# Kernel tuning notes

Measured on AMD Instinct MI355X. Metric: run time of the kernel, lower is better.

## Reference

```python
import jax, jax.numpy as jnp
import numpy as np

MEL_BINS = 128
NUM_KEYS = 88
FMAX = 8000.0
HPS_HARMONICS = 3
Q = 0.85  # threshold_percentile / 100


def _mel_frequencies(n_mels, fmin=0.0, fmax=FMAX):
    # Replicates librosa.mel_frequencies (Slaney scale, htk=False)
    f_sp = 200.0 / 3.0
    min_log_hz = 1000.0
    min_log_mel = min_log_hz / f_sp
    logstep = np.log(6.4) / 27.0

    def hz_to_mel(f):
        f = np.asarray(f, dtype=np.float64)
        lin = f / f_sp
        log = min_log_mel + np.log(np.maximum(f, 1e-12) / min_log_hz) / logstep
        return np.where(f >= min_log_hz, log, lin)

    def mel_to_hz(m):
        m = np.asarray(m, dtype=np.float64)
        lin = f_sp * m
        log = min_log_hz * np.exp(logstep * (m - min_log_mel))
        return np.where(m >= min_log_mel, log, lin)

    mels = np.linspace(hz_to_mel(fmin), hz_to_mel(fmax), n_mels)
    return mel_to_hz(mels)


def _compute_key_bins():
    mel_freqs = _mel_frequencies(MEL_BINS)
    bins = []
    for k in range(NUM_KEYS):
        freq = 440.0 * 2.0 ** ((k + 21 - 69) / 12.0)
        bin_idx = int(np.argmin(np.abs(mel_freqs - freq)))
        bins.append(min(bin_idx, MEL_BINS - 1))
    return np.asarray(bins, dtype=np.int64)


def setup_inputs() -> dict:
    key = jax.random.key(0)
    mel = jax.random.normal(key, (32, MEL_BINS, 8192), dtype=jnp.float32)
    key_bins = jnp.asarray(_compute_key_bins())
    return {"mel": mel, "key_bins": key_bins}


def reference(mel, key_bins):
    # mel: [B, MEL_BINS, T]
    spec = jnp.exp(mel)
    hps = spec
    for h in range(2, HPS_HARMONICS + 1):
        down = spec[:, ::h, :]          # [B, ceil(MEL_BINS/h), T]
        L = down.shape[1]
        hps = hps.at[:, :L, :].multiply(down)
    key_energies = hps[:, key_bins, :]  # [B, K, T]
    B, K, T = key_energies.shape
    flat = key_energies.transpose(0, 2, 1).reshape(B * T, K)
    thresh = jnp.quantile(flat, Q, axis=1, keepdims=True)  # linear interp, matches torch.quantile
    probs = (flat >= thresh).astype(jnp.float32).reshape(B, T, K).transpose(0, 2, 1)
    return (probs, probs)
```

## Files before the change

kernel.cpp:

```cpp
#include <hip/hip_runtime.h>
#include <math.h>

namespace {
constexpr int kB    = 32;
constexpr int kMel  = 128;
constexpr int kT    = 8192;
constexpr int kKeys = 88;
constexpr int kTop  = 15;
constexpr int kD    = 57;

constexpr int kDistM[kD] = {
    1,  2,  3,  4,  5,  6,  7,  8,  9, 10, 11, 12, 13, 14, 15, 16, 17,
   19, 20, 21, 22, 23, 25, 26, 28, 29, 31, 33, 35, 37, 39, 42,
   44, 46, 49, 51, 53, 56, 58, 60, 63, 65, 68, 70, 72, 75, 77, 79,
   82, 84, 86, 89, 91, 93, 96, 98, 101};
constexpr int kCnt[kD] = {
    5, 9, 6, 4, 3, 3, 3, 2, 2, 2, 1, 2, 1, 1, 1, 1, 2,
    1, 1, 1, 1, 1, 1, 1, 1, 1, 1, 1, 1, 1, 1, 1,
    1, 1, 1, 1, 1, 1, 1, 1, 1, 1, 1, 1, 1, 1, 1, 1,
    1, 1, 1, 1, 1, 1, 1, 1, 1};
constexpr int kIdx[kKeys] = {
    0, 0, 0, 0, 0,
    1, 1, 1, 1, 1, 1, 1, 1, 1,
    2, 2, 2, 2, 2, 2,
    3, 3, 3, 3,
    4, 4, 4,
    5, 5, 5,
    6, 6, 6,
    7, 7,
    8, 8,
    9, 9,
   10,
   11, 11,
   12, 13, 14, 15,
   16, 16,
   17, 18, 19, 20, 21, 22, 23, 24, 25, 26, 27, 28, 29, 30, 31,
   32, 33, 34, 35, 36, 37, 38, 39, 40, 41, 42, 43, 44, 45, 46, 47,
   48, 49, 50, 51, 52, 53, 54, 55, 56};
}

__device__ __forceinline__ void top_insert(float (&top)[kTop], float v) {
#pragma unroll
  for (int j = 0; j < kTop; ++j) {
    const float hi = fmaxf(top[j], v);
    v = fminf(top[j], v);
    top[j] = hi;
  }
}

__global__ __launch_bounds__(256, 4) void key_probs_kernel(
    const float* __restrict__ mel, const int* __restrict__ key_bins,
    float* __restrict__ out) {
  __shared__ int sbins[kKeys];
  const int tid = threadIdx.x;
  int ok = 1;
  if (tid < kKeys) {
    const int bin = key_bins[tid];
    sbins[tid] = bin;
    ok = (bin == kDistM[kIdx[tid]]);
  }
  const int allok = __syncthreads_and(ok);

  const int t = blockIdx.x * 256 + tid;
  const int b = blockIdx.y;
  const float* melb = mel + (size_t)b * kMel * kT + t;
  float* o0 = out + (size_t)b * kKeys * kT + t;
  float* o1 = o0 + (size_t)kB * kKeys * kT;

  if (allok) {
    float sd[kD];
#pragma unroll
    for (int j = 0; j < kD; ++j) {
      const int m = kDistM[j];
      float v = melb[(size_t)m * kT];
      if (2 * m < kMel) v += melb[(size_t)(2 * m) * kT];
      if (3 * m < kMel) v += melb[(size_t)(3 * m) * kT];
      sd[j] = v;
    }

    float top[kTop];
#pragma unroll
    for (int j = 0; j < kTop; ++j) top[j] = -1e30f;
#pragma unroll
    for (int j = 0; j < kD; ++j) {
#pragma unroll
      for (int c = 0; c < kCnt[j]; ++c) top_insert(top, sd[j]);
    }

    float r74 = top[13];
    const float vstar = top[13];

    int neq = 0;
    bool near_ne = false;
#pragma unroll
    for (int j = 0; j < kD; ++j) {
      const float d = sd[j] - vstar;
      const bool c = fabsf(d) < 1e-5f;
      near_ne = near_ne || (c && (d != 0.0f));
      neq += (c && (d == 0.0f)) ? 1 : 0;
    }
    const bool amb = near_ne || (neq > 1);

    if (amb) {
      float tp[kTop];
#pragma unroll
      for (int j = 0; j < kTop; ++j) tp[j] = 0.0f;
#pragma unroll
      for (int j = 0; j < kD; ++j) {
        const int m = kDistM[j];
        float v = (float)::exp((double)melb[(size_t)m * kT]);
        if (2 * m < kMel) v *= (float)::exp((double)melb[(size_t)(2 * m) * kT]);
        if (3 * m < kMel) v *= (float)::exp((double)melb[(size_t)(3 * m) * kT]);
        sd[j] = v;
#pragma unroll
        for (int c = 0; c < kCnt[j]; ++c) top_insert(tp, v);
      }
      r74 = tp[13];
    }

#pragma unroll
    for (int k = 0; k < kKeys; ++k) {
      const float r = (sd[kIdx[k]] >= r74) ? 1.0f : 0.0f;
      __builtin_nontemporal_store(r, &o0[(size_t)k * kT]);
      __builtin_nontemporal_store(r, &o1[(size_t)k * kT]);
    }
    return;
  }

  float s[kKeys];
#pragma unroll
  for (int k = 0; k < kKeys; ++k) {
    const int m = __builtin_amdgcn_readfirstlane(sbins[k]);
    const int r1 = (m < 64) ? 2 * m : m;
    const int r2 = (m < 43) ? 3 * m : m;
    const float w1 = (m < 64) ? 1.0f : 0.0f;
    const float w2 = (m < 43) ? 1.0f : 0.0f;
    const float v0 = melb[(size_t)m * kT];
    const float v1 = melb[(size_t)r1 * kT];
    const float v2 = melb[(size_t)r2 * kT];
    s[k] = v0 + w1 * v1 + w2 * v2;
  }

  float top[kTop];
#pragma unroll
  for (int j = 0; j < kTop; ++j) top[j] = -1e30f;
#pragma unroll
  for (int k = 0; k < kKeys; ++k) top_insert(top, s[k]);

  float r74 = top[13];
  const float vstar = top[13];

  bool tieok = true;
  int bmin = 0x3fffffff;
  int bmax = -0x3fffffff;
#pragma unroll
  for (int k = 0; k < kKeys; ++k) {
    const int m = __builtin_amdgcn_readfirstlane(sbins[k]);
    const float d = s[k] - vstar;
    const bool c = fabsf(d) < 1e-5f;
    tieok = tieok && (!c || (d == 0.0f));
    bmin = (c && m < bmin) ? m : bmin;
    bmax = (c && m > bmax) ? m : bmax;
  }
  const bool amb = !(tieok && (bmin == bmax));

  if (amb) {
    float tp[kTop];
#pragma unroll
    for (int j = 0; j < kTop; ++j) tp[j] = 0.0f;
#pragma unroll
    for (int k = 0; k < kKeys; ++k) {
      const int m = __builtin_amdgcn_readfirstlane(sbins[k]);
      float v = (float)::exp((double)melb[(size_t)m * kT]);
      if (m < 64) v *= (float)::exp((double)melb[(size_t)(2 * m) * kT]);
      if (m < 43) v *= (float)::exp((double)melb[(size_t)(3 * m) * kT]);
      s[k] = v;
      top_insert(tp, v);
    }
    r74 = tp[13];
  }

#pragma unroll
  for (int k = 0; k < kKeys; ++k) {
    const float r = (s[k] >= r74) ? 1.0f : 0.0f;
    __builtin_nontemporal_store(r, &o0[(size_t)k * kT]);
    __builtin_nontemporal_store(r, &o1[(size_t)k * kT]);
  }
}

extern "C" void kernel_launch(void* const* d_in, const int* in_sizes, int n_in,
                              void* d_out, int out_size, void* d_ws, size_t ws_size,
                              hipStream_t stream) {
  const float* mel = (const float*)d_in[0];
  const int* key_bins = (const int*)d_in[1];
  float* out = (float*)d_out;
  dim3 grid(kT / 256, kB);
  key_probs_kernel<<<grid, dim3(256), 0, stream>>>(mel, key_bins, out);
}
```

Baseline: 294.2 us.

## Pack threshold results with ballots into shared memory and emit vectorized float4 stores

Each wave now ballots its per-key comparison results into a shared bitmask table, and the block size grows to 1024 threads. After a block barrier, the threads expand the bits back into floats and write both output copies with 16-byte nontemporal vector stores, with each wave covering 11 output rows. This replaces per-thread 4-byte strided stores with wider stores, aiming at better write efficiency. The trade-offs are a block-wide sync and possibly lower occupancy from the 1024-thread blocks under heavy register use.

```diff
diff --git a/kernel.cpp b/kernel.cpp
--- a/kernel.cpp
+++ b/kernel.cpp
@@ -8,6 +8,12 @@
 constexpr int kKeys = 88;
 constexpr int kTop  = 15;
 constexpr int kD    = 57;
+
+constexpr int kThreads = 1024;
+constexpr int kWaves   = kThreads / 64;
+constexpr int kBlockT  = kThreads;
+
+typedef float floatx4 __attribute__((ext_vector_type(4)));
 
 constexpr int kDistM[kD] = {
     1,  2,  3,  4,  5,  6,  7,  8,  9, 10, 11, 12, 13, 14, 15, 16, 17,
@@ -48,10 +54,11 @@
   }
 }
 
-__global__ __launch_bounds__(256, 4) void key_probs_kernel(
+__global__ __launch_bounds__(kThreads, 1) void key_probs_kernel(
     const float* __restrict__ mel, const int* __restrict__ key_bins,
     float* __restrict__ out) {
   __shared__ int sbins[kKeys];
+  __shared__ unsigned long long fl[kKeys][kWaves];
   const int tid = threadIdx.x;
   int ok = 1;
   if (tid < kKeys) {
@@ -61,11 +68,10 @@
   }
   const int allok = __syncthreads_and(ok);
 
-  const int t = blockIdx.x * 256 + tid;
-  const int b = blockIdx.y;
-  const float* melb = mel + (size_t)b * kMel * kT + t;
-  float* o0 = out + (size_t)b * kKeys * kT + t;
-  float* o1 = o0 + (size_t)kB * kKeys * kT;
+  const int t0 = blockIdx.x * kBlockT;
+  const int b  = blockIdx.y;
+  const float* melb = mel + (size_t)b * kMel * kT + t0 + tid;
+  const int w = tid >> 6, lane = tid & 63;
 
   if (allok) {
     float sd[kD];
@@ -120,71 +126,91 @@
 
 #pragma unroll
     for (int k = 0; k < kKeys; ++k) {
-      const float r = (sd[kIdx[k]] >= r74) ? 1.0f : 0.0f;
-      __builtin_nontemporal_store(r, &o0[(size_t)k * kT]);
-      __builtin_nontemporal_store(r, &o1[(size_t)k * kT]);
-    }
-    return;
-  }
-
-  float s[kKeys];
-#pragma unroll
-  for (int k = 0; k < kKeys; ++k) {
-    const int m = __builtin_amdgcn_readfirstlane(sbins[k]);
-    const int r1 = (m < 64) ? 2 * m : m;
-    const int r2 = (m < 43) ? 3 * m : m;
-    const float w1 = (m < 64) ? 1.0f : 0.0f;
-    const float w2 = (m < 43) ? 1.0f : 0.0f;
-    const float v0 = melb[(size_t)m * kT];
-    const float v1 = melb[(size_t)r1 * kT];
-    const float v2 = melb[(size_t)r2 * kT];
-    s[k] = v0 + w1 * v1 + w2 * v2;
-  }
-
-  float top[kTop];
-#pragma unroll
-  for (int j = 0; j < kTop; ++j) top[j] = -1e30f;
-#pragma unroll
-  for (int k = 0; k < kKeys; ++k) top_insert(top, s[k]);
-
-  float r74 = top[13];
-  const float vstar = top[13];
-
-  bool tieok = true;
-  int bmin = 0x3fffffff;
-  int bmax = -0x3fffffff;
-#pragma unroll
-  for (int k = 0; k < kKeys; ++k) {
-    const int m = __builtin_amdgcn_readfirstlane(sbins[k]);
-    const float d = s[k] - vstar;
-    const bool c = fabsf(d) < 1e-5f;
-    tieok = tieok && (!c || (d == 0.0f));
-    bmin = (c && m < bmin) ? m : bmin;
-    bmax = (c && m > bmax) ? m : bmax;
-  }
-  const bool amb = !(tieok && (bmin == bmax));
-
-  if (amb) {
-    float tp[kTop];
-#pragma unroll
-    for (int j = 0; j < kTop; ++j) tp[j] = 0.0f;
+      const unsigned long long m = __ballot(sd[kIdx[k]] >= r74);
+      if (lane == 0) fl[k][w] = m;
+    }
+  } else {
+    float s[kKeys];
 #pragma unroll
     for (int k = 0; k < kKeys; ++k) {
       const int m = __builtin_amdgcn_readfirstlane(sbins[k]);
-      float v = (float)::exp((double)melb[(size_t)m * kT]);
-      if (m < 64) v *= (float)::exp((double)melb[(size_t)(2 * m) * kT]);
-      if (m < 43) v *= (float)::exp((double)melb[(size_t)(3 * m) * kT]);
-      s[k] = v;
-      top_insert(tp, v);
-    }
-    r74 = tp[13];
-  }
-
-#pragma unroll
-  for (int k = 0; k < kKeys; ++k) {
-    const float r = (s[k] >= r74) ? 1.0f : 0.0f;
-    __builtin_nontemporal_store(r, &o0[(size_t)k * kT]);
-    __builtin_nontemporal_store(r, &o1[(size_t)k * kT]);
+      const int r1 = (m < 64) ? 2 * m : m;
+      const int r2 = (m < 43) ? 3 * m : m;
+      const float w1 = (m < 64) ? 1.0f : 0.0f;
+      const float w2 = (m < 43) ? 1.0f : 0.0f;
+      const float v0 = melb[(size_t)m * kT];
+      const float v1 = melb[(size_t)r1 * kT];
+      const float v2 = melb[(size_t)r2 * kT];
+      s[k] = v0 + w1 * v1 + w2 * v2;
+    }
+
+    float top[kTop];
+#pragma unroll
+    for (int j = 0; j < kTop; ++j) top[j] = -1e30f;
+#pragma unroll
+    for (int k = 0; k < kKeys; ++k) top_insert(top, s[k]);
+
+    float r74 = top[13];
+    const float vstar = top[13];
+
+    bool tieok = true;
+    int bmin = 0x3fffffff;
+    int bmax = -0x3fffffff;
+#pragma unroll
+    for (int k = 0; k < kKeys; ++k) {
+      const int m = __builtin_amdgcn_readfirstlane(sbins[k]);
+      const float d = s[k] - vstar;
+      const bool c = fabsf(d) < 1e-5f;
+      tieok = tieok && (!c || (d == 0.0f));
+      bmin = (c && m < bmin) ? m : bmin;
+      bmax = (c && m > bmax) ? m : bmax;
+    }
+    const bool amb = !(tieok && (bmin == bmax));
+
+    if (amb) {
+      float tp[kTop];
+#pragma unroll
+      for (int j = 0; j < kTop; ++j) tp[j] = 0.0f;
+#pragma unroll
+      for (int k = 0; k < kKeys; ++k) {
+        const int m = __builtin_amdgcn_readfirstlane(sbins[k]);
+        float v = (float)::exp((double)melb[(size_t)m * kT]);
+        if (m < 64) v *= (float)::exp((double)melb[(size_t)(2 * m) * kT]);
+        if (m < 43) v *= (float)::exp((double)melb[(size_t)(3 * m) * kT]);
+        s[k] = v;
+        top_insert(tp, v);
+      }
+      r74 = tp[13];
+    }
+
+#pragma unroll
+    for (int k = 0; k < kKeys; ++k) {
+      const unsigned long long m = __ballot(s[k] >= r74);
+      if (lane == 0) fl[k][w] = m;
+    }
+  }
+
+  __syncthreads();
+
+  float* ob = out + (size_t)b * kKeys * kT + t0;
+  const size_t copyStride = (size_t)kB * kKeys * kT;
+#pragma unroll
+  for (int rr = 0; rr < 11; ++rr) {
+    const int r = w * 11 + rr;
+    const int k = (r < kKeys) ? r : r - kKeys;
+    float* dst = ob + ((r < kKeys) ? 0 : copyStride) + (size_t)k * kT;
+#pragma unroll
+    for (int i = 0; i < 4; ++i) {
+      const unsigned long long word = fl[k][i * 4 + (lane >> 4)];
+      const int sh = (lane & 15) * 4;
+      const unsigned bits = (unsigned)(word >> sh) & 0xFu;
+      floatx4 v;
+      v.x = (bits & 1u) ? 1.0f : 0.0f;
+      v.y = (bits & 2u) ? 1.0f : 0.0f;
+      v.z = (bits & 4u) ? 1.0f : 0.0f;
+      v.w = (bits & 8u) ? 1.0f : 0.0f;
+      __builtin_nontemporal_store(v, (floatx4*)(dst + i * 256 + lane * 4));
+    }
   }
 }
 
@@ -194,6 +220,6 @@
   const float* mel = (const float*)d_in[0];
   const int* key_bins = (const int*)d_in[1];
   float* out = (float*)d_out;
-  dim3 grid(kT / 256, kB);
-  key_probs_kernel<<<grid, dim3(256), 0, stream>>>(mel, key_bins, out);
-}
+  dim3 grid(kT / kBlockT, kB);
+  key_probs_kernel<<<grid, dim3(kThreads), 0, stream>>>(mel, key_bins, out);
+}
```

Measured after the change: 299.5 us. About the same (+1.8%).
